# Performance work log

Measured on AMD Instinct MI355X. Metric: run time of the kernel, lower is better.

## Reference

```python
import jax, jax.numpy as jnp
import numpy as np
from jax import lax


def _conv1d(x, w, b):
    # x: [B, C_in, L], w: [C_out, C_in, 3], 'same' padding
    y = lax.conv_general_dilated(x, w, window_strides=(1,), padding=[(1, 1)],
                                 dimension_numbers=('NCH', 'OIH', 'NCH'))
    return y + b[None, :, None]


def _bn(x, g, beta, mean, var, eps=1e-5):
    # BatchNorm1d in inference mode (running stats)
    scale = (g / jnp.sqrt(var + eps))[None, :, None]
    return (x - mean[None, :, None]) * scale + beta[None, :, None]


def setup_inputs() -> dict:
    key = jax.random.key(0)
    ks = jax.random.split(key, 24)
    B, L, C = 16, 8192, 256
    d = {}
    d['x'] = jax.random.normal(ks[0], (B, 1, L), dtype=jnp.float32)
    d['sc'] = 4
    d['fs'] = 16000
    # conv_fw_1: Conv1d(1, 256)
    d['w_in'] = jax.random.normal(ks[1], (C, 1, 3), dtype=jnp.float32) * 0.05
    d['b_in'] = jax.random.normal(ks[2], (C,), dtype=jnp.float32) * 0.05
    d['w_r1'] = jax.random.normal(ks[3], (C, C, 3), dtype=jnp.float32) * 0.02
    d['b_r1'] = jax.random.normal(ks[4], (C,), dtype=jnp.float32) * 0.05
    d['g1'] = 1.0 + 0.1 * jax.random.normal(ks[5], (C,), dtype=jnp.float32)
    d['be1'] = jax.random.normal(ks[6], (C,), dtype=jnp.float32) * 0.05
    d['m1'] = jax.random.normal(ks[7], (C,), dtype=jnp.float32) * 0.05
    d['v1'] = jax.random.uniform(ks[8], (C,), dtype=jnp.float32, minval=0.5, maxval=1.5)
    d['w_r2'] = jax.random.normal(ks[9], (C, C, 3), dtype=jnp.float32) * 0.02
    d['b_r2'] = jax.random.normal(ks[10], (C,), dtype=jnp.float32) * 0.05
    d['g2'] = 1.0 + 0.1 * jax.random.normal(ks[11], (C,), dtype=jnp.float32)
    d['be2'] = jax.random.normal(ks[12], (C,), dtype=jnp.float32) * 0.05
    d['m2'] = jax.random.normal(ks[13], (C,), dtype=jnp.float32) * 0.05
    d['v2'] = jax.random.uniform(ks[14], (C,), dtype=jnp.float32, minval=0.5, maxval=1.5)
    # up_sample: up_block1 Conv1d(256,256), up_block22 Conv1d(256,4)
    d['w_u1'] = jax.random.normal(ks[15], (C, C, 3), dtype=jnp.float32) * 0.02
    d['b_u1'] = jax.random.normal(ks[16], (C,), dtype=jnp.float32) * 0.05
    d['w_u2'] = jax.random.normal(ks[17], (4, C, 3), dtype=jnp.float32) * 0.02
    d['b_u2'] = jax.random.normal(ks[18], (4,), dtype=jnp.float32) * 0.05
    return d


def reference(x, sc, fs, w_in, b_in, w_r1, b_r1, g1, be1, m1, v1,
              w_r2, b_r2, g2, be2, m2, v2, w_u1, b_u1, w_u2, b_u2):
    SCALE = 0.15  # residual scale used in FDRN.forward
    R = 4         # FDRN.forward hard-codes Up(x, 4)
    h = jax.nn.relu(_conv1d(x, w_in, b_in))  # [B,256,L]

    def resblock(h):
        r = _bn(_conv1d(h, w_r1, b_r1), g1, be1, m1, v1)
        r = jax.nn.relu(r)
        r = _bn(_conv1d(r, w_r2, b_r2), g2, be2, m2, v2)
        return h + r * SCALE

    # same Resblock module applied 32 times (shared weights)
    h = lax.fori_loop(0, 32, lambda i, hh: resblock(hh), h)

    h = jax.nn.relu(_conv1d(h, w_u1, b_u1))   # [B,256,L]
    h = jax.nn.relu(_conv1d(h, w_u2, b_u2))   # [B,4,L]
    # _pharse_shift(I, r): New[i,0,j] = I[i, j % r, j // r]  ==  transpose + reshape
    B, C, L = h.shape
    h = jnp.transpose(h, (0, 2, 1)).reshape(B, 1, L * C)  # C == R == 4
    return jax.nn.relu(h)
```

## Files before the change

kernel.cpp:

```cpp
#include <hip/hip_runtime.h>

typedef _Float16 half8 __attribute__((ext_vector_type(8)));
typedef _Float16 half4 __attribute__((ext_vector_type(4)));
typedef __fp16 fp16x2 __attribute__((ext_vector_type(2)));
typedef float floatx4 __attribute__((ext_vector_type(4)));
typedef unsigned int uintx4 __attribute__((ext_vector_type(4)));

#define CCH 256
#define LSEQ 8192
#define LTILE 128
#define AROWS 132
#define NT 64
#define ROWB 512
#define LDSB (AROWS * ROWB)

__device__ __forceinline__ int swz(int row, int byte) {
  return row * ROWB + (byte ^ ((row & 7) << 4));
}
__device__ __forceinline__ floatx4 zero4() {
  floatx4 v; v[0] = 0.f; v[1] = 0.f; v[2] = 0.f; v[3] = 0.f; return v;
}
__device__ __forceinline__ unsigned long long pack4(float y0, float y1, float y2, float y3) {
  fp16x2 lo = __builtin_amdgcn_cvt_pkrtz(y0, y1);
  fp16x2 hi = __builtin_amdgcn_cvt_pkrtz(y2, y3);
  unsigned ulo = __builtin_bit_cast(unsigned, lo);
  unsigned uhi = __builtin_bit_cast(unsigned, hi);
  return (unsigned long long)ulo | ((unsigned long long)uhi << 32);
}

template <int MODE>
__global__ __launch_bounds__(512, 1) void res6(
    const _Float16* __restrict__ src, _Float16* __restrict__ dst,
    const _Float16* __restrict__ wA, const _Float16* __restrict__ wB,
    const float* __restrict__ sc1v, const float* __restrict__ sh1v,
    const float* __restrict__ sc2v, const float* __restrict__ sh2v) {
  __shared__ __align__(16) char smem[LDSB];
  const int t = threadIdx.x;
  const int bx = blockIdx.x;
  const int b = bx >> 6;
  const int tile = bx & (NT - 1);
  const int l0 = tile * LTILE;

  for (int c = t; c < AROWS * 32; c += 512) {
    const int row = c >> 5, col = c & 31;
    const int l = l0 + row - 2;
    uintx4 v = {0u, 0u, 0u, 0u};
    if (l >= 0 && l < LSEQ)
      v = *(const uintx4*)(src + (((size_t)b * LSEQ + l) << 8) + col * 8);
    *(uintx4*)(smem + swz(row, col * 16)) = v;
  }
  __syncthreads();

  const int w = t >> 6, ln = t & 63;
  const int cg = w >> 1, lgrp = w & 1;
  const int lrow = ln & 15, kgrp = ln >> 4;
  const size_t wbase = (size_t)(cg * 64 + lrow) * 32 + kgrp * 8;

  if constexpr (MODE == 0) {
    const int jtb = lgrp * 5;
    const int njt = lgrp ? 4 : 5;
    floatx4 acc[4][5];
#pragma unroll
    for (int i = 0; i < 4; ++i)
#pragma unroll
      for (int j = 0; j < 5; ++j) acc[i][j] = zero4();
    {
      const _Float16* wp = wA + wbase;
      half8 a0 = *(const half8*)(wp);
      half8 a1 = *(const half8*)(wp + 16 * 32);
      half8 a2 = *(const half8*)(wp + 32 * 32);
      half8 a3 = *(const half8*)(wp + 48 * 32);
      for (int it = 0; it < 24; ++it) {
        const int nit = (it < 23) ? it + 1 : it;
        const _Float16* np = wA + (size_t)nit * (CCH * 32) + wbase;
        half8 n0 = *(const half8*)(np);
        half8 n1 = *(const half8*)(np + 16 * 32);
        half8 n2 = *(const half8*)(np + 32 * 32);
        half8 n3 = *(const half8*)(np + 48 * 32);
        const int tap = it >> 3, kc = it & 7;
        const int byt = kc * 64 + kgrp * 16;
        __builtin_amdgcn_s_setprio(1);
#pragma unroll
        for (int jj = 0; jj < 5; ++jj) {
          if (jj < njt) {
            int arow = (jtb + jj) * 16 + lrow + tap;
            if (arow > AROWS - 1) arow = AROWS - 1;
            half8 bf = *(const half8*)(smem + swz(arow, byt));
            acc[0][jj] = __builtin_amdgcn_mfma_f32_16x16x32_f16(a0, bf, acc[0][jj], 0, 0, 0);
            acc[1][jj] = __builtin_amdgcn_mfma_f32_16x16x32_f16(a1, bf, acc[1][jj], 0, 0, 0);
            acc[2][jj] = __builtin_amdgcn_mfma_f32_16x16x32_f16(a2, bf, acc[2][jj], 0, 0, 0);
            acc[3][jj] = __builtin_amdgcn_mfma_f32_16x16x32_f16(a3, bf, acc[3][jj], 0, 0, 0);
          }
        }
        __builtin_amdgcn_s_setprio(0);
        a0 = n0; a1 = n1; a2 = n2; a3 = n3;
      }
    }
    __syncthreads();
#pragma unroll
    for (int i = 0; i < 4; ++i) {
      const int co = cg * 64 + i * 16 + kgrp * 4;
      floatx4 s = *(const floatx4*)(sc1v + co);
      floatx4 sh = *(const floatx4*)(sh1v + co);
#pragma unroll
      for (int jj = 0; jj < 5; ++jj) {
        if (jj < njt) {
          const int r = (jtb + jj) * 16 + lrow;
          if (r < 130) {
            const int l = l0 - 1 + r;
            const float m = ((l >= 0) && (l < LSEQ)) ? 1.f : 0.f;
            unsigned long long pk = pack4(
                fmaxf(acc[i][jj][0] * s[0] + sh[0], 0.f) * m,
                fmaxf(acc[i][jj][1] * s[1] + sh[1], 0.f) * m,
                fmaxf(acc[i][jj][2] * s[2] + sh[2], 0.f) * m,
                fmaxf(acc[i][jj][3] * s[3] + sh[3], 0.f) * m);
            *(unsigned long long*)(smem + swz(r, co * 2)) = pk;
          }
        }
      }
    }
    __syncthreads();
    floatx4 acc2[4][4];
#pragma unroll
    for (int i = 0; i < 4; ++i)
#pragma unroll
      for (int j = 0; j < 4; ++j) acc2[i][j] = zero4();
    {
      const _Float16* wp = wB + wbase;
      half8 a0 = *(const half8*)(wp);
      half8 a1 = *(const half8*)(wp + 16 * 32);
      half8 a2 = *(const half8*)(wp + 32 * 32);
      half8 a3 = *(const half8*)(wp + 48 * 32);
      for (int it = 0; it < 24; ++it) {
        const int nit = (it < 23) ? it + 1 : it;
        const _Float16* np = wB + (size_t)nit * (CCH * 32) + wbase;
        half8 n0 = *(const half8*)(np);
        half8 n1 = *(const half8*)(np + 16 * 32);
        half8 n2 = *(const half8*)(np + 32 * 32);
        half8 n3 = *(const half8*)(np + 48 * 32);
        const int tap = it >> 3, kc = it & 7;
        const int byt = kc * 64 + kgrp * 16;
        __builtin_amdgcn_s_setprio(1);
#pragma unroll
        for (int j = 0; j < 4; ++j) {
          const int brow = (lgrp * 4 + j) * 16 + lrow + tap;
          half8 bf = *(const half8*)(smem + swz(brow, byt));
          acc2[0][j] = __builtin_amdgcn_mfma_f32_16x16x32_f16(a0, bf, acc2[0][j], 0, 0, 0);
          acc2[1][j] = __builtin_amdgcn_mfma_f32_16x16x32_f16(a1, bf, acc2[1][j], 0, 0, 0);
          acc2[2][j] = __builtin_amdgcn_mfma_f32_16x16x32_f16(a2, bf, acc2[2][j], 0, 0, 0);
          acc2[3][j] = __builtin_amdgcn_mfma_f32_16x16x32_f16(a3, bf, acc2[3][j], 0, 0, 0);
        }
        __builtin_amdgcn_s_setprio(0);
        a0 = n0; a1 = n1; a2 = n2; a3 = n3;
      }
    }
#pragma unroll
    for (int i = 0; i < 4; ++i) {
      const int co = cg * 64 + i * 16 + kgrp * 4;
      floatx4 s = *(const floatx4*)(sc2v + co);
      floatx4 sh = *(const floatx4*)(sh2v + co);
#pragma unroll
      for (int j = 0; j < 4; ++j) {
        const int v = (lgrp * 4 + j) * 16 + lrow;
        const int l = l0 + v;
        const size_t off = (((size_t)b * LSEQ + l) << 8) + co;
        half4 h = *(const half4*)(src + off);
        unsigned long long pk = pack4(
            (float)h[0] + 0.15f * (acc2[i][j][0] * s[0] + sh[0]),
            (float)h[1] + 0.15f * (acc2[i][j][1] * s[1] + sh[1]),
            (float)h[2] + 0.15f * (acc2[i][j][2] * s[2] + sh[2]),
            (float)h[3] + 0.15f * (acc2[i][j][3] * s[3] + sh[3]));
        *(unsigned long long*)(dst + off) = pk;
      }
    }
  } else {
    floatx4 acc[4][4];
#pragma unroll
    for (int i = 0; i < 4; ++i)
#pragma unroll
      for (int j = 0; j < 4; ++j) acc[i][j] = zero4();
    for (int it = 0; it < 24; ++it) {
      const int tap = it >> 3, kc = it & 7;
      const _Float16* wp = wA + (size_t)it * (CCH * 32) + wbase;
      half8 a0 = *(const half8*)(wp);
      half8 a1 = *(const half8*)(wp + 16 * 32);
      half8 a2 = *(const half8*)(wp + 32 * 32);
      half8 a3 = *(const half8*)(wp + 48 * 32);
      const int byt = kc * 64 + kgrp * 16;
#pragma unroll
      for (int j = 0; j < 4; ++j) {
        const int arow = (lgrp * 4 + j) * 16 + lrow + 1 + tap;
        half8 bf = *(const half8*)(smem + swz(arow, byt));
        acc[0][j] = __builtin_amdgcn_mfma_f32_16x16x32_f16(a0, bf, acc[0][j], 0, 0, 0);
        acc[1][j] = __builtin_amdgcn_mfma_f32_16x16x32_f16(a1, bf, acc[1][j], 0, 0, 0);
        acc[2][j] = __builtin_amdgcn_mfma_f32_16x16x32_f16(a2, bf, acc[2][j], 0, 0, 0);
        acc[3][j] = __builtin_amdgcn_mfma_f32_16x16x32_f16(a3, bf, acc[3][j], 0, 0, 0);
      }
    }
#pragma unroll
    for (int i = 0; i < 4; ++i) {
      const int co = cg * 64 + i * 16 + kgrp * 4;
      floatx4 s = *(const floatx4*)(sc1v + co);
      floatx4 sh = *(const floatx4*)(sh1v + co);
#pragma unroll
      for (int j = 0; j < 4; ++j) {
        const int v = (lgrp * 4 + j) * 16 + lrow;
        const int l = l0 + v;
        unsigned long long pk = pack4(
            fmaxf(acc[i][j][0] * s[0] + sh[0], 0.f),
            fmaxf(acc[i][j][1] * s[1] + sh[1], 0.f),
            fmaxf(acc[i][j][2] * s[2] + sh[2], 0.f),
            fmaxf(acc[i][j][3] * s[3] + sh[3], 0.f));
        *(unsigned long long*)(dst + (((size_t)b * LSEQ + l) << 8) + co) = pk;
      }
    }
  }
}

__global__ void conv_in_kernel(const float* __restrict__ x, const float* __restrict__ w_in,
                               const float* __restrict__ b_in, _Float16* __restrict__ hout) {
  size_t idx = (size_t)blockIdx.x * blockDim.x + threadIdx.x;
  int co = (int)(idx & 255);
  size_t pos = idx >> 8;
  int l = (int)(pos & (LSEQ - 1));
  int b = (int)(pos >> 13);
  float acc = b_in[co];
#pragma unroll
  for (int k = 0; k < 3; ++k) {
    int lg = l + k - 1;
    if (lg >= 0 && lg < LSEQ) acc += w_in[co * 3 + k] * x[(size_t)b * LSEQ + lg];
  }
  hout[idx] = (_Float16)fmaxf(acc, 0.f);
}

__global__ __launch_bounds__(256) void conv_u2_kernel(
    const _Float16* __restrict__ hin, const float* __restrict__ w2T4 ,
    const float* __restrict__ b_u2, float* __restrict__ out) {
  const size_t idx = (size_t)blockIdx.x * 256 + threadIdx.x;
  const int l = (int)(idx & (LSEQ - 1));
  const int b = (int)(idx >> 13);
  floatx4 acc = *(const floatx4*)b_u2;
  for (int tap = 0; tap < 3; ++tap) {
    const int lg = l + tap - 1;
    if (lg < 0 || lg >= LSEQ) continue;
    const half8* hp = (const half8*)(hin + (((size_t)b * LSEQ + lg) << 8));
    const floatx4* wp = (const floatx4*)(w2T4 + tap * 1024);
    for (int q = 0; q < 32; ++q) {
      half8 hv = hp[q];
#pragma unroll
      for (int r = 0; r < 8; ++r) {
        floatx4 wv = wp[q * 8 + r];
        float h = (float)hv[r];
        acc[0] += h * wv[0]; acc[1] += h * wv[1]; acc[2] += h * wv[2]; acc[3] += h * wv[3];
      }
    }
  }
  floatx4 y;
#pragma unroll
  for (int r = 0; r < 4; ++r) y[r] = fmaxf(acc[r], 0.f);
  *(floatx4*)(out + ((size_t)b << 15) + (size_t)l * 4) = y;
}

__global__ void prep_kernel(
    const float* __restrict__ w_r1, const float* __restrict__ w_r2,
    const float* __restrict__ w_u1, const float* __restrict__ w_u2,
    const float* __restrict__ b_r1, const float* __restrict__ g1,
    const float* __restrict__ be1, const float* __restrict__ m1, const float* __restrict__ v1,
    const float* __restrict__ b_r2, const float* __restrict__ g2,
    const float* __restrict__ be2, const float* __restrict__ m2, const float* __restrict__ v2,
    const float* __restrict__ b_u1,
    _Float16* __restrict__ wT1, _Float16* __restrict__ wT2, _Float16* __restrict__ wTu1,
    float* __restrict__ wu2T4,
    float* __restrict__ sc1, float* __restrict__ sh1,
    float* __restrict__ sc2, float* __restrict__ sh2,
    float* __restrict__ scu1, float* __restrict__ shu1) {
  int idx = blockIdx.x * blockDim.x + threadIdx.x;
  if (idx < 3 * CCH * CCH) {
    int tap = idx >> 16;
    int rem = idx & 65535;
    int kc = rem >> 13;
    int rem2 = rem & 8191;
    int co = rem2 >> 5, c = rem2 & 31;
    int ci = kc * 32 + c;
    size_t s = ((size_t)co * CCH + ci) * 3 + tap;
    wT1[idx] = (_Float16)w_r1[s];
    wT2[idx] = (_Float16)w_r2[s];
    wTu1[idx] = (_Float16)w_u1[s];
  }
  if (idx < 3 * CCH * 4) {
    int co = idx & 3;
    int ci = (idx >> 2) & 255;
    int tap = idx >> 10;
    wu2T4[idx] = w_u2[((size_t)co * CCH + ci) * 3 + tap];
  }
  if (idx < CCH) {
    float s1 = g1[idx] * rsqrtf(v1[idx] + 1e-5f);
    sc1[idx] = s1;
    sh1[idx] = (b_r1[idx] - m1[idx]) * s1 + be1[idx];
    float s2 = g2[idx] * rsqrtf(v2[idx] + 1e-5f);
    sc2[idx] = s2;
    sh2[idx] = (b_r2[idx] - m2[idx]) * s2 + be2[idx];
    scu1[idx] = 1.f;
    shu1[idx] = b_u1[idx];
  }
}

__global__ void diag_kernel(float* out, float v) { out[0] = v; }

extern "C" void kernel_launch(void* const* d_in, const int* in_sizes, int n_in,
                              void* d_out, int out_size, void* d_ws, size_t ws_size,
                              hipStream_t stream) {
  (void)in_sizes; (void)n_in; (void)out_size;
  const size_t HELEMS = (size_t)16 * LSEQ * CCH;
  const size_t HB = HELEMS * sizeof(_Float16);
  const size_t NEED = 2 * HB + 2u * 1024 * 1024;
  if (ws_size < NEED) {
    diag_kernel<<<1, 1, 0, stream>>>((float*)d_out, 1000.0f + (float)(ws_size >> 20));
    return;
  }
  const float* x    = (const float*)d_in[0];
  const float* w_in = (const float*)d_in[3];
  const float* b_in = (const float*)d_in[4];
  const float* w_r1 = (const float*)d_in[5];
  const float* b_r1 = (const float*)d_in[6];
  const float* g1   = (const float*)d_in[7];
  const float* be1  = (const float*)d_in[8];
  const float* m1   = (const float*)d_in[9];
  const float* v1   = (const float*)d_in[10];
  const float* w_r2 = (const float*)d_in[11];
  const float* b_r2 = (const float*)d_in[12];
  const float* g2   = (const float*)d_in[13];
  const float* be2  = (const float*)d_in[14];
  const float* m2   = (const float*)d_in[15];
  const float* v2   = (const float*)d_in[16];
  const float* w_u1 = (const float*)d_in[17];
  const float* b_u1 = (const float*)d_in[18];
  const float* w_u2 = (const float*)d_in[19];
  const float* b_u2 = (const float*)d_in[20];

  char* ws = (char*)d_ws;
  _Float16* buf0 = (_Float16*)ws;
  _Float16* buf1 = (_Float16*)(ws + HB);
  _Float16* wT1  = (_Float16*)(ws + 2 * HB);
  _Float16* wT2  = wT1 + 3 * CCH * CCH;
  _Float16* wTu1 = wT2 + 3 * CCH * CCH;
  float* sc1  = (float*)(wTu1 + 3 * CCH * CCH);
  float* sh1  = sc1 + CCH;
  float* sc2  = sh1 + CCH;
  float* sh2  = sc2 + CCH;
  float* scu1 = sh2 + CCH;
  float* shu1 = scu1 + CCH;
  float* wu2T4 = shu1 + CCH;

  prep_kernel<<<768, 256, 0, stream>>>(w_r1, w_r2, w_u1, w_u2, b_r1, g1, be1, m1, v1,
                                       b_r2, g2, be2, m2, v2, b_u1,
                                       wT1, wT2, wTu1, wu2T4, sc1, sh1, sc2, sh2, scu1, shu1);
  conv_in_kernel<<<131072, 256, 0, stream>>>(x, w_in, b_in, buf0);
  const int grid = 16 * NT;
  for (int k = 0; k < 32; ++k) {
    const _Float16* s = (k & 1) ? buf1 : buf0;
    _Float16* d = (k & 1) ? buf0 : buf1;
    res6<0><<<grid, 512, 0, stream>>>(s, d, wT1, wT2, sc1, sh1, sc2, sh2);
  }
  res6<1><<<grid, 512, 0, stream>>>(buf0, buf1, wTu1, (const _Float16*)nullptr,
                                    scu1, shu1, (const float*)nullptr, (const float*)nullptr);
  conv_u2_kernel<<<512, 256, 0, stream>>>(buf1, wu2T4, b_u2, (float*)d_out);
}
```

Baseline: 4.643 ms.

## Fold residual and BN2 shift into conv2 accumulator init, read residual from LDS

```diff
diff --git a/kernel.cpp b/kernel.cpp
--- a/kernel.cpp
+++ b/kernel.cpp
@@ -29,11 +29,12 @@
 }
 
 template <int MODE>
-__global__ __launch_bounds__(512, 1) void res6(
+__global__ __launch_bounds__(512, 1) void res7(
     const _Float16* __restrict__ src, _Float16* __restrict__ dst,
     const _Float16* __restrict__ wA, const _Float16* __restrict__ wB,
     const float* __restrict__ sc1v, const float* __restrict__ sh1v,
-    const float* __restrict__ sc2v, const float* __restrict__ sh2v) {
+    const float* __restrict__ sc2pv, const float* __restrict__ rs2v,
+    const float* __restrict__ tshv) {
   __shared__ __align__(16) char smem[LDSB];
   const int t = threadIdx.x;
   const int bx = blockIdx.x;
@@ -96,7 +97,7 @@
         a0 = n0; a1 = n1; a2 = n2; a3 = n3;
       }
     }
-    __syncthreads();
+    unsigned long long pk1[4][5];
 #pragma unroll
     for (int i = 0; i < 4; ++i) {
       const int co = cg * 64 + i * 16 + kgrp * 4;
@@ -109,22 +110,44 @@
           if (r < 130) {
             const int l = l0 - 1 + r;
             const float m = ((l >= 0) && (l < LSEQ)) ? 1.f : 0.f;
-            unsigned long long pk = pack4(
+            pk1[i][jj] = pack4(
                 fmaxf(acc[i][jj][0] * s[0] + sh[0], 0.f) * m,
                 fmaxf(acc[i][jj][1] * s[1] + sh[1], 0.f) * m,
                 fmaxf(acc[i][jj][2] * s[2] + sh[2], 0.f) * m,
                 fmaxf(acc[i][jj][3] * s[3] + sh[3], 0.f) * m);
-            *(unsigned long long*)(smem + swz(r, co * 2)) = pk;
           }
         }
       }
     }
+    floatx4 c2[4][4];
+#pragma unroll
+    for (int i = 0; i < 4; ++i) {
+      const int co = cg * 64 + i * 16 + kgrp * 4;
+      floatx4 rs = *(const floatx4*)(rs2v + co);
+      floatx4 ts = *(const floatx4*)(tshv + co);
+#pragma unroll
+      for (int j = 0; j < 4; ++j) {
+        const int v = (lgrp * 4 + j) * 16 + lrow;
+        half4 h = *(const half4*)(smem + swz(v + 2, co * 2));
+#pragma unroll
+        for (int q = 0; q < 4; ++q)
+          c2[i][j][q] = (float)h[q] * rs[q] + ts[q];
+      }
+    }
     __syncthreads();
-    floatx4 acc2[4][4];
-#pragma unroll
-    for (int i = 0; i < 4; ++i)
-#pragma unroll
-      for (int j = 0; j < 4; ++j) acc2[i][j] = zero4();
+#pragma unroll
+    for (int i = 0; i < 4; ++i) {
+      const int co = cg * 64 + i * 16 + kgrp * 4;
+#pragma unroll
+      for (int jj = 0; jj < 5; ++jj) {
+        if (jj < njt) {
+          const int r = (jtb + jj) * 16 + lrow;
+          if (r < 130)
+            *(unsigned long long*)(smem + swz(r, co * 2)) = pk1[i][jj];
+        }
+      }
+    }
+    __syncthreads();
     {
       const _Float16* wp = wB + wbase;
       half8 a0 = *(const half8*)(wp);
@@ -145,10 +168,10 @@
         for (int j = 0; j < 4; ++j) {
           const int brow = (lgrp * 4 + j) * 16 + lrow + tap;
           half8 bf = *(const half8*)(smem + swz(brow, byt));
-          acc2[0][j] = __builtin_amdgcn_mfma_f32_16x16x32_f16(a0, bf, acc2[0][j], 0, 0, 0);
-          acc2[1][j] = __builtin_amdgcn_mfma_f32_16x16x32_f16(a1, bf, acc2[1][j], 0, 0, 0);
-          acc2[2][j] = __builtin_amdgcn_mfma_f32_16x16x32_f16(a2, bf, acc2[2][j], 0, 0, 0);
-          acc2[3][j] = __builtin_amdgcn_mfma_f32_16x16x32_f16(a3, bf, acc2[3][j], 0, 0, 0);
+          c2[0][j] = __builtin_amdgcn_mfma_f32_16x16x32_f16(a0, bf, c2[0][j], 0, 0, 0);
+          c2[1][j] = __builtin_amdgcn_mfma_f32_16x16x32_f16(a1, bf, c2[1][j], 0, 0, 0);
+          c2[2][j] = __builtin_amdgcn_mfma_f32_16x16x32_f16(a2, bf, c2[2][j], 0, 0, 0);
+          c2[3][j] = __builtin_amdgcn_mfma_f32_16x16x32_f16(a3, bf, c2[3][j], 0, 0, 0);
         }
         __builtin_amdgcn_s_setprio(0);
         a0 = n0; a1 = n1; a2 = n2; a3 = n3;
@@ -157,20 +180,17 @@
 #pragma unroll
     for (int i = 0; i < 4; ++i) {
       const int co = cg * 64 + i * 16 + kgrp * 4;
-      floatx4 s = *(const floatx4*)(sc2v + co);
-      floatx4 sh = *(const floatx4*)(sh2v + co);
+      floatx4 sp = *(const floatx4*)(sc2pv + co);
 #pragma unroll
       for (int j = 0; j < 4; ++j) {
         const int v = (lgrp * 4 + j) * 16 + lrow;
         const int l = l0 + v;
         const size_t off = (((size_t)b * LSEQ + l) << 8) + co;
-        half4 h = *(const half4*)(src + off);
-        unsigned long long pk = pack4(
-            (float)h[0] + 0.15f * (acc2[i][j][0] * s[0] + sh[0]),
-            (float)h[1] + 0.15f * (acc2[i][j][1] * s[1] + sh[1]),
-            (float)h[2] + 0.15f * (acc2[i][j][2] * s[2] + sh[2]),
-            (float)h[3] + 0.15f * (acc2[i][j][3] * s[3] + sh[3]));
-        *(unsigned long long*)(dst + off) = pk;
+        half4 o;
+#pragma unroll
+        for (int q = 0; q < 4; ++q)
+          o[q] = (_Float16)(c2[i][j][q] * sp[q]);
+        *(half4*)(dst + off) = o;
       }
     }
   } else {
@@ -272,7 +292,7 @@
     _Float16* __restrict__ wT1, _Float16* __restrict__ wT2, _Float16* __restrict__ wTu1,
     float* __restrict__ wu2T4,
     float* __restrict__ sc1, float* __restrict__ sh1,
-    float* __restrict__ sc2, float* __restrict__ sh2,
+    float* __restrict__ sc2p, float* __restrict__ rs2, float* __restrict__ tsh,
     float* __restrict__ scu1, float* __restrict__ shu1) {
   int idx = blockIdx.x * blockDim.x + threadIdx.x;
   if (idx < 3 * CCH * CCH) {
@@ -298,8 +318,11 @@
     sc1[idx] = s1;
     sh1[idx] = (b_r1[idx] - m1[idx]) * s1 + be1[idx];
     float s2 = g2[idx] * rsqrtf(v2[idx] + 1e-5f);
-    sc2[idx] = s2;
-    sh2[idx] = (b_r2[idx] - m2[idx]) * s2 + be2[idx];
+    float sh2 = (b_r2[idx] - m2[idx]) * s2 + be2[idx];
+    float sp = 0.15f * s2;
+    sc2p[idx] = sp;
+    rs2[idx] = 1.0f / sp;
+    tsh[idx] = sh2 / s2;
     scu1[idx] = 1.f;
     shu1[idx] = b_u1[idx];
   }
@@ -346,23 +369,26 @@
   _Float16* wTu1 = wT2 + 3 * CCH * CCH;
   float* sc1  = (float*)(wTu1 + 3 * CCH * CCH);
   float* sh1  = sc1 + CCH;
-  float* sc2  = sh1 + CCH;
-  float* sh2  = sc2 + CCH;
-  float* scu1 = sh2 + CCH;
+  float* sc2p = sh1 + CCH;
+  float* rs2  = sc2p + CCH;
+  float* tsh  = rs2 + CCH;
+  float* scu1 = tsh + CCH;
   float* shu1 = scu1 + CCH;
   float* wu2T4 = shu1 + CCH;
 
   prep_kernel<<<768, 256, 0, stream>>>(w_r1, w_r2, w_u1, w_u2, b_r1, g1, be1, m1, v1,
                                        b_r2, g2, be2, m2, v2, b_u1,
-                                       wT1, wT2, wTu1, wu2T4, sc1, sh1, sc2, sh2, scu1, shu1);
+                                       wT1, wT2, wTu1, wu2T4, sc1, sh1, sc2p, rs2, tsh,
+                                       scu1, shu1);
   conv_in_kernel<<<131072, 256, 0, stream>>>(x, w_in, b_in, buf0);
   const int grid = 16 * NT;
   for (int k = 0; k < 32; ++k) {
     const _Float16* s = (k & 1) ? buf1 : buf0;
     _Float16* d = (k & 1) ? buf0 : buf1;
-    res6<0><<<grid, 512, 0, stream>>>(s, d, wT1, wT2, sc1, sh1, sc2, sh2);
-  }
-  res6<1><<<grid, 512, 0, stream>>>(buf0, buf1, wTu1, (const _Float16*)nullptr,
-                                    scu1, shu1, (const float*)nullptr, (const float*)nullptr);
+    res7<0><<<grid, 512, 0, stream>>>(s, d, wT1, wT2, sc1, sh1, sc2p, rs2, tsh);
+  }
+  res7<1><<<grid, 512, 0, stream>>>(buf0, buf1, wTu1, (const _Float16*)nullptr,
+                                    scu1, shu1, (const float*)nullptr,
+                                    (const float*)nullptr, (const float*)nullptr);
   conv_u2_kernel<<<512, 256, 0, stream>>>(buf1, wu2T4, b_u2, (float*)d_out);
 }
```

Measured after the change: 4.375 ms. 1.06x faster.
